# Kernel tuning notes

Hardware: AMD Instinct MI355X
Metric: run time of the kernel (lower is better)

Reference implementation:

```python
import jax, jax.numpy as jnp
import numpy as np

B, N, D = 16, 2048, 1024   # batch, num_windows, input_dim
H, A = 256, 128            # feature head dim, attention hidden dim
EPS = 1e-5                 # torch LayerNorm eps
NEG = -1e9                 # finite mask value (avoids NaN in softmax/grads)
KMAX = max(1, N // 10)     # static upper bound on per-sample top-k


def setup_inputs() -> dict:
    key = jax.random.key(0)
    ks = jax.random.split(key, 6)
    rn = lambda k, shape, sc: jax.random.normal(k, shape, jnp.float32) * sc
    return {
        "x": rn(ks[0], (B, N, D), 1.0),
        "lengths": jax.random.randint(ks[1], (B,), 0, N, dtype=jnp.int64)
                   if jax.config.jax_enable_x64 else
                   jax.random.randint(ks[1], (B,), 0, N, dtype=jnp.int32),
        # feature_head: Linear(D,H) + LayerNorm(H) (+ GELU, dropout=eval no-op)
        "W1": rn(ks[2], (H, D), D ** -0.5), "b1": jnp.zeros((H,), jnp.float32),
        "ln_g": jnp.ones((H,), jnp.float32), "ln_b": jnp.zeros((H,), jnp.float32),
        # attention: Linear(H,A) -> tanh -> Linear(A,1)
        "Wa1": rn(ks[3], (A, H), H ** -0.5), "ba1": jnp.zeros((A,), jnp.float32),
        "Wa2": rn(ks[4], (1, A), A ** -0.5), "ba2": jnp.zeros((1,), jnp.float32),
        # classifier: Linear(H,1)
        "Wc": rn(ks[5], (1, H), H ** -0.5), "bc": jnp.zeros((1,), jnp.float32),
    }


def reference(x, lengths, W1, b1, ln_g, ln_b, Wa1, ba1, Wa2, ba2, Wc, bc):
    # feature head: Linear + LayerNorm + exact GELU (dropout is identity in eval)
    h = jnp.einsum('bnd,hd->bnh', x, W1) + b1
    mu = h.mean(-1, keepdims=True)
    var = h.var(-1, keepdims=True)  # biased, as in torch LayerNorm
    h = (h - mu) * jax.lax.rsqrt(var + EPS) * ln_g + ln_b
    h = jax.nn.gelu(h, approximate=False)

    instance_scores = jnp.einsum('bnh,oh->bno', h, Wc)[..., 0] + bc[0]   # (B, N)
    a_hidden = jnp.tanh(jnp.einsum('bnh,ah->bna', h, Wa1) + ba1)
    attn_logits = jnp.einsum('bna,oa->bno', a_hidden, Wa2)[..., 0] + ba2[0]  # (B, N)

    T = lengths                                    # (B,)
    mask = jnp.arange(N)[None, :] < T[:, None]     # (B, N) valid-window mask

    # masked softmax attention pooling over the first T windows
    w = jax.nn.softmax(jnp.where(mask, attn_logits, NEG), axis=1)
    attn_score = jnp.sum(w * instance_scores * mask, axis=1)

    # dynamic top-k: k = max(1, floor(0.1*T)); take static KMAX then mask ranks
    k_i = jnp.maximum(1, T // 10)                  # (B,)
    vals, _ = jax.lax.top_k(jnp.where(mask, instance_scores, NEG), KMAX)
    rank_mask = jnp.arange(KMAX)[None, :] < k_i[:, None]
    topk_mean = jnp.sum(vals * rank_mask, axis=1) / k_i.astype(vals.dtype)

    video = jnp.where(T > 0, 0.5 * attn_score + 0.5 * topk_mean,
                      jnp.zeros((), vals.dtype))
    return video[:, None], instance_scores
```

## Files before the change

kernel.cpp:

```cpp
#include <hip/hip_runtime.h>
#include <hip/hip_bf16.h>
#include <cmath>

#define Bn 16
#define Nn 2048
#define Dn 1024
#define Hn 256
#define An 128

typedef __bf16 bf16x8 __attribute__((ext_vector_type(8)));
typedef float f32x4 __attribute__((ext_vector_type(4)));
typedef unsigned short ushort8v __attribute__((ext_vector_type(8)));
typedef unsigned int uint4v __attribute__((ext_vector_type(4)));

#define LDS_BARRIER do {                                   \
    asm volatile("s_waitcnt lgkmcnt(0)" ::: "memory");     \
    __builtin_amdgcn_s_barrier();                          \
    __builtin_amdgcn_sched_barrier(0);                     \
  } while (0)

static __device__ __forceinline__ unsigned short f2bf(float f) {
  unsigned u = __float_as_uint(f);
  u += 0x7fffu + ((u >> 16) & 1u);
  return (unsigned short)(u >> 16);
}

static __device__ __forceinline__ bf16x8 cvt8(const float4 a, const float4 b) {
  bf16x8 r;
  r[0] = (__bf16)a.x; r[1] = (__bf16)a.y; r[2] = (__bf16)a.z; r[3] = (__bf16)a.w;
  r[4] = (__bf16)b.x; r[5] = (__bf16)b.y; r[6] = (__bf16)b.z; r[7] = (__bf16)b.w;
  return r;
}

__global__ __launch_bounds__(256) void pack_weights(
    const float* __restrict__ W1, const float* __restrict__ Wa1,
    unsigned short* __restrict__ w1p, unsigned short* __restrict__ wa1p) {
  const int idx = blockIdx.x * 256 + threadIdx.x;
  const float* src;
  unsigned short* dst;
  if (blockIdx.x < 128) {
    const int kc  = idx >> 10;
    const int u   = idx & 1023;
    const int col = u >> 2;
    const int lq  = (u & 3) ^ ((col >> 1) & 3);
    src = W1 + (size_t)col * Dn + (kc << 5) + (lq << 3);
    dst = w1p + (size_t)idx * 8;
  } else {
    const int v   = idx - 32768;
    const int row = v >> 5;
    const int ls  = (v & 31) ^ (row & 7);
    src = Wa1 + (size_t)row * Hn + (ls << 3);
    dst = wa1p + (size_t)v * 8;
  }
  const float4 a = *(const float4*)src;
  const float4 b = *(const float4*)(src + 4);
  ushort8v o;
  o[0] = f2bf(a.x); o[1] = f2bf(a.y); o[2] = f2bf(a.z); o[3] = f2bf(a.w);
  o[4] = f2bf(b.x); o[5] = f2bf(b.y); o[6] = f2bf(b.z); o[7] = f2bf(b.w);
  *(ushort8v*)dst = o;
}

#define K1A(p) ((p) * 4096)
#define K1B(p) (8192 + (p) * 16384)
#define K1H    8192
#define K1RED  40960
__global__ __launch_bounds__(256, 3) void gemm_ln_kernel(
    const float* __restrict__ x,
    const float* __restrict__ b1,
    const float* __restrict__ ln_g,
    const float* __restrict__ ln_b,
    const float* __restrict__ Wc,
    const float* __restrict__ bc,
    const unsigned short* __restrict__ w1p,
    float* __restrict__ scores_out,
    unsigned short* __restrict__ h_out)
{
  __shared__ __align__(16) char lds[43008];

  const int tid  = threadIdx.x;
  const int wv   = tid >> 6;
  const int lane = tid & 63;
  const int l15  = lane & 15;
  const int lhi  = lane >> 4;
  const int rg   = wv >> 1;
  const int cw   = wv & 1;

  const int gr0 = blockIdx.x << 6;
  const int bb  = gr0 >> 11;
  const int n0  = gr0 & (Nn - 1);

  f32x4 acc[2][8];
  #pragma unroll
  for (int rf = 0; rf < 2; ++rf)
    #pragma unroll
    for (int cf = 0; cf < 8; ++cf)
      acc[rf][cf] = (f32x4){0.f, 0.f, 0.f, 0.f};

  const int arow = tid >> 2, aq = tid & 3;
  const int aphys = aq ^ ((arow >> 1) & 3);
  const float* xsrc = x + (size_t)(gr0 + arow) * Dn + (aq << 3);
  const int awoff = arow * 64 + (aphys << 4);

  const unsigned short* bsrc = w1p + (size_t)tid * 8;

  const int bx    = lhi ^ ((l15 >> 1) & 3);
  const int aoff  = ((rg << 5) + l15) * 64 + (bx << 4);
  const int boff  = (((cw << 7) + l15) * 64) + (bx << 4);

  float4 xs0, xs1;
  uint4v Bst[4];

  auto loadStage = [&](int kc) {
    xs0 = *(const float4*)(xsrc + (kc << 5));
    xs1 = *(const float4*)(xsrc + (kc << 5) + 4);
    const unsigned short* bp = bsrc + (size_t)kc * 8192;
    #pragma unroll
    for (int q = 0; q < 4; ++q)
      Bst[q] = *(const uint4v*)(bp + q * 2048);
  };
  auto writeStage = [&](int p) {
    *(bf16x8*)(lds + K1A(p) + awoff) = cvt8(xs0, xs1);
    #pragma unroll
    for (int q = 0; q < 4; ++q)
      *(uint4v*)(lds + K1B(p) + ((q << 8) + tid) * 16) = Bst[q];
  };
  auto computeStep = [&](int p) {
    const char* Ab = lds + K1A(p);
    const char* Bb = lds + K1B(p);
    __builtin_amdgcn_s_setprio(1);
    const bf16x8 aA = *(const bf16x8*)(Ab + aoff);
    const bf16x8 aB = *(const bf16x8*)(Ab + aoff + 1024);
    #pragma unroll
    for (int cf = 0; cf < 8; ++cf) {
      const bf16x8 bfr = *(const bf16x8*)(Bb + boff + cf * 1024);
      acc[0][cf] = __builtin_amdgcn_mfma_f32_16x16x32_bf16(aA, bfr, acc[0][cf], 0, 0, 0);
      acc[1][cf] = __builtin_amdgcn_mfma_f32_16x16x32_bf16(aB, bfr, acc[1][cf], 0, 0, 0);
    }
    __builtin_amdgcn_s_setprio(0);
  };

  loadStage(0);
  writeStage(0);
  LDS_BARRIER;

  #pragma unroll
  for (int kc = 0; kc < 32; ++kc) {
    const int p = kc & 1;
    if (kc < 31) loadStage(kc + 1);
    computeStep(p);
    if (kc < 31) {
      writeStage(p ^ 1);
      LDS_BARRIER;
    }
  }
  __syncthreads();

  float (*red)[8] = (float(*)[8])(lds + K1RED);

  const float bc0 = bc[0];
  float b1v[8];
  #pragma unroll
  for (int cf = 0; cf < 8; ++cf) b1v[cf] = b1[(cw << 7) + (cf << 4) + l15];

  float ps[2][4], ps2[2][4];
  #pragma unroll
  for (int rf = 0; rf < 2; ++rf)
    #pragma unroll
    for (int r = 0; r < 4; ++r) { ps[rf][r] = 0.f; ps2[rf][r] = 0.f; }

  #pragma unroll
  for (int rf = 0; rf < 2; ++rf)
    #pragma unroll
    for (int cf = 0; cf < 8; ++cf)
      #pragma unroll
      for (int r = 0; r < 4; ++r) {
        const float v = acc[rf][cf][r] + b1v[cf];
        acc[rf][cf][r] = v;
        ps[rf][r] += v; ps2[rf][r] += v * v;
      }
  #pragma unroll
  for (int rf = 0; rf < 2; ++rf)
    #pragma unroll
    for (int r = 0; r < 4; ++r)
      #pragma unroll
      for (int s = 1; s < 16; s <<= 1) {
        ps[rf][r]  += __shfl_xor(ps[rf][r],  s, 64);
        ps2[rf][r] += __shfl_xor(ps2[rf][r], s, 64);
      }
  if (l15 == 0) {
    #pragma unroll
    for (int rf = 0; rf < 2; ++rf)
      #pragma unroll
      for (int r = 0; r < 4; ++r) {
        const int rowb = (rg << 5) + (rf << 4) + (lhi << 2) + r;
        red[rowb][cw << 1]       = ps[rf][r];
        red[rowb][(cw << 1) + 1] = ps2[rf][r];
      }
  }
  __syncthreads();

  float mu[2][4], inv[2][4];
  #pragma unroll
  for (int rf = 0; rf < 2; ++rf)
    #pragma unroll
    for (int r = 0; r < 4; ++r) {
      const int rowb = (rg << 5) + (rf << 4) + (lhi << 2) + r;
      const float s = red[rowb][0] + red[rowb][2];
      const float q = red[rowb][1] + red[rowb][3];
      const float m = s * (1.f / 256.f);
      const float var = q * (1.f / 256.f) - m * m;
      mu[rf][r] = m;
      inv[rf][r] = rsqrtf(var + 1e-5f);
    }

  float gv[8], bv[8], wcv[8];
  #pragma unroll
  for (int cf = 0; cf < 8; ++cf) {
    const int col = (cw << 7) + (cf << 4) + l15;
    gv[cf] = ln_g[col]; bv[cf] = ln_b[col]; wcv[cf] = Wc[col];
  }
  float sc[2][4];
  #pragma unroll
  for (int rf = 0; rf < 2; ++rf)
    #pragma unroll
    for (int r = 0; r < 4; ++r) sc[rf][r] = 0.f;

  #pragma unroll
  for (int rf = 0; rf < 2; ++rf)
    #pragma unroll
    for (int cf = 0; cf < 8; ++cf)
      #pragma unroll
      for (int r = 0; r < 4; ++r) {
        float v = (acc[rf][cf][r] - mu[rf][r]) * inv[rf][r] * gv[cf] + bv[cf];
        v = 0.5f * v * (1.f + erff(v * 0.70710678118654752f));
        sc[rf][r] += v * wcv[cf];
        const int rowb = (rg << 5) + (rf << 4) + (lhi << 2) + r;
        const int col  = (cw << 7) + (cf << 4) + l15;
        *(__bf16*)(lds + K1H + rowb * 512 + (((col >> 3) ^ (rowb & 7)) << 4)
                   + ((col & 7) << 1)) = (__bf16)v;
      }
  #pragma unroll
  for (int rf = 0; rf < 2; ++rf)
    #pragma unroll
    for (int r = 0; r < 4; ++r)
      #pragma unroll
      for (int s = 1; s < 16; s <<= 1)
        sc[rf][r] += __shfl_xor(sc[rf][r], s, 64);
  if (l15 == 0) {
    #pragma unroll
    for (int rf = 0; rf < 2; ++rf)
      #pragma unroll
      for (int r = 0; r < 4; ++r) {
        const int rowb = (rg << 5) + (rf << 4) + (lhi << 2) + r;
        red[rowb][4 + cw] = sc[rf][r];
      }
  }
  __syncthreads();
  if (tid < 64)
    scores_out[(size_t)bb * Nn + n0 + tid] = red[tid][4] + red[tid][5] + bc0;

  #pragma unroll
  for (int j = 0; j < 8; ++j) {
    const int g   = (j << 8) + tid;
    const int row = g >> 5;
    const int c   = g & 31;
    const bf16x8 hv = *(const bf16x8*)(lds + K1H + row * 512 +
                                       ((c ^ (row & 7)) << 4));
    *(bf16x8*)(h_out + (size_t)(gr0 + row) * 256 + (c << 3)) = hv;
  }
}

__global__ __launch_bounds__(512) void stage2_kernel(
    const unsigned short* __restrict__ h_in,
    const unsigned short* __restrict__ wa1p,
    const float* __restrict__ ba1,
    const float* __restrict__ Wa2,
    const float* __restrict__ ba2,
    float* __restrict__ logits_out)
{
  __shared__ __align__(16) char lds2[65536];

  const int tid  = threadIdx.x;
  const int wv   = tid >> 6;
  const int lane = tid & 63;
  const int l15  = lane & 15;
  const int lhi  = lane >> 4;

  const int gr0 = blockIdx.x << 7;
  const int bb  = gr0 >> 11;
  const int n0  = gr0 & (Nn - 1);

  {
    uint4v st[8];
    #pragma unroll
    for (int j = 0; j < 8; ++j)
      st[j] = *(const uint4v*)(wa1p + (size_t)((j << 9) + tid) * 8);
    #pragma unroll
    for (int j = 0; j < 8; ++j)
      *(uint4v*)(lds2 + ((j << 9) + tid) * 16) = st[j];
  }
  __syncthreads();

  f32x4 acc2[8];
  #pragma unroll
  for (int cf = 0; cf < 8; ++cf) acc2[cf] = (f32x4){0.f, 0.f, 0.f, 0.f};

  const unsigned short* hrow = h_in + (size_t)(gr0 + (wv << 4) + l15) * 256 + (lhi << 3);
  #pragma unroll
  for (int ks = 0; ks < 8; ++ks) {
    const bf16x8 af = *(const bf16x8*)(hrow + (ks << 5));
    #pragma unroll
    for (int cf = 0; cf < 8; ++cf) {
      const int row2 = (cf << 4) + l15;
      const bf16x8 bfr = *(const bf16x8*)(lds2 + row2 * 512 +
                          ((((ks << 2) + lhi) ^ (row2 & 7)) << 4));
      acc2[cf] = __builtin_amdgcn_mfma_f32_16x16x32_bf16(af, bfr, acc2[cf], 0, 0, 0);
    }
  }
  const float ba20 = ba2[0];
  float lg[4] = {0.f, 0.f, 0.f, 0.f};
  #pragma unroll
  for (int cf = 0; cf < 8; ++cf) {
    const int col = (cf << 4) + l15;
    const float bav = ba1[col], w2v = Wa2[col];
    #pragma unroll
    for (int r = 0; r < 4; ++r) {
      const float t = acc2[cf][r] + bav;
      const float e = __expf(2.f * t);
      const float th = 1.f - 2.f / (e + 1.f);
      lg[r] += th * w2v;
    }
  }
  #pragma unroll
  for (int r = 0; r < 4; ++r)
    #pragma unroll
    for (int s = 1; s < 16; s <<= 1) lg[r] += __shfl_xor(lg[r], s, 64);
  if (l15 == 0) {
    #pragma unroll
    for (int r = 0; r < 4; ++r)
      logits_out[(size_t)bb * Nn + n0 + (wv << 4) + (lhi << 2) + r] = lg[r] + ba20;
  }
}

__global__ __launch_bounds__(256) void finalize_kernel(
    const int* __restrict__ lengths,
    const float* __restrict__ scores,
    const float* __restrict__ logits,
    float* __restrict__ video)
{
  const int b = blockIdx.x;
  const int tid = threadIdx.x;
  __shared__ float sS[Nn];
  __shared__ float sL[Nn];
  __shared__ unsigned skey[Nn];
  __shared__ float sred[8];

  const int T = lengths[b];
  for (int i = tid; i < Nn; i += 256) {
    sS[i] = scores[(size_t)b * Nn + i];
    sL[i] = logits[(size_t)b * Nn + i];
  }
  __syncthreads();
  if (T <= 0) { if (tid == 0) video[b] = 0.f; return; }

  float m = -3.0e38f;
  for (int i = tid; i < T; i += 256) m = fmaxf(m, sL[i]);
  #pragma unroll
  for (int s = 1; s < 64; s <<= 1) m = fmaxf(m, __shfl_xor(m, s, 64));
  if ((tid & 63) == 0) sred[tid >> 6] = m;
  __syncthreads();
  m = fmaxf(fmaxf(sred[0], sred[1]), fmaxf(sred[2], sred[3]));
  __syncthreads();

  float se = 0.f, swe = 0.f;
  for (int i = tid; i < T; i += 256) {
    const float e = expf(sL[i] - m);
    se += e; swe += e * sS[i];
  }
  #pragma unroll
  for (int s = 1; s < 64; s <<= 1) { se += __shfl_xor(se, s, 64); swe += __shfl_xor(swe, s, 64); }
  if ((tid & 63) == 0) { sred[tid >> 6] = se; sred[4 + (tid >> 6)] = swe; }
  __syncthreads();
  se  = sred[0] + sred[1] + sred[2] + sred[3];
  swe = sred[4] + sred[5] + sred[6] + sred[7];
  __syncthreads();
  const float attn = swe / se;

  for (int i = tid; i < T; i += 256) {
    const unsigned u = __float_as_uint(sS[i]);
    skey[i] = (u & 0x80000000u) ? ~u : (u | 0x80000000u);
  }
  __syncthreads();
  const int k = max(1, T / 10);
  unsigned ans = 0u;
  for (int bit = 31; bit >= 0; --bit) {
    const unsigned cand = ans | (1u << bit);
    int c = 0;
    for (int i = tid; i < T; i += 256) c += (skey[i] >= cand) ? 1 : 0;
    #pragma unroll
    for (int s = 1; s < 64; s <<= 1) c += __shfl_xor(c, s, 64);
    if ((tid & 63) == 0) sred[tid >> 6] = (float)c;
    __syncthreads();
    c = (int)(sred[0] + sred[1] + sred[2] + sred[3]);
    __syncthreads();
    if (c >= k) ans = cand;
  }
  int cgt = 0; float sgt = 0.f;
  for (int i = tid; i < T; i += 256) {
    if (skey[i] > ans) { cgt++; sgt += sS[i]; }
  }
  #pragma unroll
  for (int s = 1; s < 64; s <<= 1) { cgt += __shfl_xor(cgt, s, 64); sgt += __shfl_xor(sgt, s, 64); }
  if ((tid & 63) == 0) { sred[tid >> 6] = (float)cgt; sred[4 + (tid >> 6)] = sgt; }
  __syncthreads();
  cgt = (int)(sred[0] + sred[1] + sred[2] + sred[3]);
  sgt = sred[4] + sred[5] + sred[6] + sred[7];

  const unsigned ub = (ans & 0x80000000u) ? (ans ^ 0x80000000u) : ~ans;
  const float kth = __uint_as_float(ub);
  const float topk = (sgt + (float)(k - cgt) * kth) / (float)k;
  if (tid == 0) video[b] = 0.5f * attn + 0.5f * topk;
}

extern "C" void kernel_launch(void* const* d_in, const int* in_sizes, int n_in,
                              void* d_out, int out_size, void* d_ws, size_t ws_size,
                              hipStream_t stream) {
  const float* x    = (const float*)d_in[0];
  const int*   len  = (const int*)  d_in[1];
  const float* W1   = (const float*)d_in[2];
  const float* b1   = (const float*)d_in[3];
  const float* ln_g = (const float*)d_in[4];
  const float* ln_b = (const float*)d_in[5];
  const float* Wa1  = (const float*)d_in[6];
  const float* ba1  = (const float*)d_in[7];
  const float* Wa2  = (const float*)d_in[8];
  const float* ba2  = (const float*)d_in[9];
  const float* Wc   = (const float*)d_in[10];
  const float* bc   = (const float*)d_in[11];

  float* out    = (float*)d_out;
  float* video  = out;
  float* scores = out + Bn;

  char* ws = (char*)d_ws;
  float*          logits = (float*)ws;
  unsigned short* h_g    = (unsigned short*)(ws + 131072);
  unsigned short* w1p    = (unsigned short*)(ws + 131072 + 16777216);
  unsigned short* wa1p   = (unsigned short*)(ws + 131072 + 16777216 + 524288);

  hipLaunchKernelGGL(pack_weights, dim3(144), dim3(256), 0, stream, W1, Wa1, w1p, wa1p);
  hipLaunchKernelGGL(gemm_ln_kernel, dim3(Bn * Nn / 64), dim3(256), 0, stream,
                     x, b1, ln_g, ln_b, Wc, bc, w1p, scores, h_g);
  hipLaunchKernelGGL(stage2_kernel, dim3(Bn * Nn / 128), dim3(512), 0, stream,
                     h_g, wa1p, ba1, Wa2, ba2, logits);
  hipLaunchKernelGGL(finalize_kernel, dim3(Bn), dim3(256), 0, stream, len, scores, logits, video);
}
```

Measured before the change: 87.40 us.

## Split GEMM+LayerNorm tile across 8 waves with one row fragment each

The fused GEMM+LayerNorm kernel goes from 256 to 512 threads per 64-row block. Each wave now owns 16 rows by 128 columns instead of 32 by 128, and staging loads are split across twice as many threads with smaller per-thread loads. The aim is to cut accumulator registers per thread so more waves fit per CU and hide global and LDS latency better. In exchange, each loaded A fragment is reused across half as many MFMAs, so LDS traffic per MFMA rises, and the per-k-step barrier now synchronises more waves.

```diff
diff --git a/kernel.cpp b/kernel.cpp
--- a/kernel.cpp
+++ b/kernel.cpp
@@ -9,6 +9,7 @@
 #define An 128
 
 typedef __bf16 bf16x8 __attribute__((ext_vector_type(8)));
+typedef __bf16 bf16x4 __attribute__((ext_vector_type(4)));
 typedef float f32x4 __attribute__((ext_vector_type(4)));
 typedef unsigned short ushort8v __attribute__((ext_vector_type(8)));
 typedef unsigned int uint4v __attribute__((ext_vector_type(4)));
@@ -23,13 +24,6 @@
   unsigned u = __float_as_uint(f);
   u += 0x7fffu + ((u >> 16) & 1u);
   return (unsigned short)(u >> 16);
-}
-
-static __device__ __forceinline__ bf16x8 cvt8(const float4 a, const float4 b) {
-  bf16x8 r;
-  r[0] = (__bf16)a.x; r[1] = (__bf16)a.y; r[2] = (__bf16)a.z; r[3] = (__bf16)a.w;
-  r[4] = (__bf16)b.x; r[5] = (__bf16)b.y; r[6] = (__bf16)b.z; r[7] = (__bf16)b.w;
-  return r;
 }
 
 __global__ __launch_bounds__(256) void pack_weights(
@@ -64,7 +58,7 @@
 #define K1B(p) (8192 + (p) * 16384)
 #define K1H    8192
 #define K1RED  40960
-__global__ __launch_bounds__(256, 3) void gemm_ln_kernel(
+__global__ __launch_bounds__(512, 4) void gemm_ln_kernel(
     const float* __restrict__ x,
     const float* __restrict__ b1,
     const float* __restrict__ ln_g,
@@ -83,58 +77,53 @@
   const int l15  = lane & 15;
   const int lhi  = lane >> 4;
   const int rg   = wv >> 1;
-  const int cw   = wv & 1;
+  const int ch   = wv & 1;
 
   const int gr0 = blockIdx.x << 6;
   const int bb  = gr0 >> 11;
   const int n0  = gr0 & (Nn - 1);
 
-  f32x4 acc[2][8];
-  #pragma unroll
-  for (int rf = 0; rf < 2; ++rf)
-    #pragma unroll
-    for (int cf = 0; cf < 8; ++cf)
-      acc[rf][cf] = (f32x4){0.f, 0.f, 0.f, 0.f};
-
-  const int arow = tid >> 2, aq = tid & 3;
-  const int aphys = aq ^ ((arow >> 1) & 3);
-  const float* xsrc = x + (size_t)(gr0 + arow) * Dn + (aq << 3);
-  const int awoff = arow * 64 + (aphys << 4);
+  f32x4 acc[8];
+  #pragma unroll
+  for (int cf = 0; cf < 8; ++cf) acc[cf] = (f32x4){0.f, 0.f, 0.f, 0.f};
+
+  const int arow = tid >> 3, aslot = tid & 7;
+  const float* xsrc = x + (size_t)(gr0 + arow) * Dn + (aslot << 2);
+  const int awoff = arow * 64 + ((((aslot >> 1) ^ ((arow >> 1) & 3)) << 4)
+                                 | ((aslot & 1) << 3));
 
   const unsigned short* bsrc = w1p + (size_t)tid * 8;
 
-  const int bx    = lhi ^ ((l15 >> 1) & 3);
-  const int aoff  = ((rg << 5) + l15) * 64 + (bx << 4);
-  const int boff  = (((cw << 7) + l15) * 64) + (bx << 4);
-
-  float4 xs0, xs1;
-  uint4v Bst[4];
+  const int arow_r = (rg << 4) + l15;
+  const int aoff   = arow_r * 64 + ((lhi ^ ((arow_r >> 1) & 3)) << 4);
+  const int boff   = (((ch << 7) + l15) * 64) + ((lhi ^ ((l15 >> 1) & 3)) << 4);
+
+  float4 xs;
+  uint4v Bst[2];
 
   auto loadStage = [&](int kc) {
-    xs0 = *(const float4*)(xsrc + (kc << 5));
-    xs1 = *(const float4*)(xsrc + (kc << 5) + 4);
+    xs = *(const float4*)(xsrc + (kc << 5));
     const unsigned short* bp = bsrc + (size_t)kc * 8192;
-    #pragma unroll
-    for (int q = 0; q < 4; ++q)
-      Bst[q] = *(const uint4v*)(bp + q * 2048);
+    Bst[0] = *(const uint4v*)(bp);
+    Bst[1] = *(const uint4v*)(bp + 4096);
   };
   auto writeStage = [&](int p) {
-    *(bf16x8*)(lds + K1A(p) + awoff) = cvt8(xs0, xs1);
-    #pragma unroll
-    for (int q = 0; q < 4; ++q)
-      *(uint4v*)(lds + K1B(p) + ((q << 8) + tid) * 16) = Bst[q];
+    bf16x4 t;
+    t[0] = (__bf16)xs.x; t[1] = (__bf16)xs.y;
+    t[2] = (__bf16)xs.z; t[3] = (__bf16)xs.w;
+    *(bf16x4*)(lds + K1A(p) + awoff) = t;
+    *(uint4v*)(lds + K1B(p) + tid * 16) = Bst[0];
+    *(uint4v*)(lds + K1B(p) + 8192 + tid * 16) = Bst[1];
   };
   auto computeStep = [&](int p) {
     const char* Ab = lds + K1A(p);
     const char* Bb = lds + K1B(p);
     __builtin_amdgcn_s_setprio(1);
     const bf16x8 aA = *(const bf16x8*)(Ab + aoff);
-    const bf16x8 aB = *(const bf16x8*)(Ab + aoff + 1024);
     #pragma unroll
     for (int cf = 0; cf < 8; ++cf) {
       const bf16x8 bfr = *(const bf16x8*)(Bb + boff + cf * 1024);
-      acc[0][cf] = __builtin_amdgcn_mfma_f32_16x16x32_bf16(aA, bfr, acc[0][cf], 0, 0, 0);
-      acc[1][cf] = __builtin_amdgcn_mfma_f32_16x16x32_bf16(aB, bfr, acc[1][cf], 0, 0, 0);
+      acc[cf] = __builtin_amdgcn_mfma_f32_16x16x32_bf16(aA, bfr, acc[cf], 0, 0, 0);
     }
     __builtin_amdgcn_s_setprio(0);
   };
@@ -160,108 +149,83 @@
   const float bc0 = bc[0];
   float b1v[8];
   #pragma unroll
-  for (int cf = 0; cf < 8; ++cf) b1v[cf] = b1[(cw << 7) + (cf << 4) + l15];
-
-  float ps[2][4], ps2[2][4];
-  #pragma unroll
-  for (int rf = 0; rf < 2; ++rf)
-    #pragma unroll
-    for (int r = 0; r < 4; ++r) { ps[rf][r] = 0.f; ps2[rf][r] = 0.f; }
-
-  #pragma unroll
-  for (int rf = 0; rf < 2; ++rf)
-    #pragma unroll
-    for (int cf = 0; cf < 8; ++cf)
-      #pragma unroll
-      for (int r = 0; r < 4; ++r) {
-        const float v = acc[rf][cf][r] + b1v[cf];
-        acc[rf][cf][r] = v;
-        ps[rf][r] += v; ps2[rf][r] += v * v;
-      }
-  #pragma unroll
-  for (int rf = 0; rf < 2; ++rf)
-    #pragma unroll
-    for (int r = 0; r < 4; ++r)
-      #pragma unroll
-      for (int s = 1; s < 16; s <<= 1) {
-        ps[rf][r]  += __shfl_xor(ps[rf][r],  s, 64);
-        ps2[rf][r] += __shfl_xor(ps2[rf][r], s, 64);
-      }
+  for (int cf = 0; cf < 8; ++cf) b1v[cf] = b1[(ch << 7) + (cf << 4) + l15];
+
+  float ps[4] = {0, 0, 0, 0}, ps2[4] = {0, 0, 0, 0};
+  #pragma unroll
+  for (int cf = 0; cf < 8; ++cf)
+    #pragma unroll
+    for (int r = 0; r < 4; ++r) {
+      const float v = acc[cf][r] + b1v[cf];
+      acc[cf][r] = v;
+      ps[r] += v; ps2[r] += v * v;
+    }
+  #pragma unroll
+  for (int r = 0; r < 4; ++r)
+    #pragma unroll
+    for (int s = 1; s < 16; s <<= 1) {
+      ps[r]  += __shfl_xor(ps[r],  s, 64);
+      ps2[r] += __shfl_xor(ps2[r], s, 64);
+    }
   if (l15 == 0) {
     #pragma unroll
-    for (int rf = 0; rf < 2; ++rf)
-      #pragma unroll
-      for (int r = 0; r < 4; ++r) {
-        const int rowb = (rg << 5) + (rf << 4) + (lhi << 2) + r;
-        red[rowb][cw << 1]       = ps[rf][r];
-        red[rowb][(cw << 1) + 1] = ps2[rf][r];
-      }
-  }
-  __syncthreads();
-
-  float mu[2][4], inv[2][4];
-  #pragma unroll
-  for (int rf = 0; rf < 2; ++rf)
-    #pragma unroll
     for (int r = 0; r < 4; ++r) {
-      const int rowb = (rg << 5) + (rf << 4) + (lhi << 2) + r;
-      const float s = red[rowb][0] + red[rowb][2];
-      const float q = red[rowb][1] + red[rowb][3];
-      const float m = s * (1.f / 256.f);
-      const float var = q * (1.f / 256.f) - m * m;
-      mu[rf][r] = m;
-      inv[rf][r] = rsqrtf(var + 1e-5f);
-    }
+      const int rowb = (rg << 4) + (lhi << 2) + r;
+      red[rowb][ch << 1]       = ps[r];
+      red[rowb][(ch << 1) + 1] = ps2[r];
+    }
+  }
+  __syncthreads();
+
+  float mu[4], inv[4];
+  #pragma unroll
+  for (int r = 0; r < 4; ++r) {
+    const int rowb = (rg << 4) + (lhi << 2) + r;
+    const float s = red[rowb][0] + red[rowb][2];
+    const float q = red[rowb][1] + red[rowb][3];
+    const float m = s * (1.f / 256.f);
+    const float var = q * (1.f / 256.f) - m * m;
+    mu[r] = m;
+    inv[r] = rsqrtf(var + 1e-5f);
+  }
 
   float gv[8], bv[8], wcv[8];
   #pragma unroll
   for (int cf = 0; cf < 8; ++cf) {
-    const int col = (cw << 7) + (cf << 4) + l15;
+    const int col = (ch << 7) + (cf << 4) + l15;
     gv[cf] = ln_g[col]; bv[cf] = ln_b[col]; wcv[cf] = Wc[col];
   }
-  float sc[2][4];
-  #pragma unroll
-  for (int rf = 0; rf < 2; ++rf)
-    #pragma unroll
-    for (int r = 0; r < 4; ++r) sc[rf][r] = 0.f;
-
-  #pragma unroll
-  for (int rf = 0; rf < 2; ++rf)
-    #pragma unroll
-    for (int cf = 0; cf < 8; ++cf)
-      #pragma unroll
-      for (int r = 0; r < 4; ++r) {
-        float v = (acc[rf][cf][r] - mu[rf][r]) * inv[rf][r] * gv[cf] + bv[cf];
-        v = 0.5f * v * (1.f + erff(v * 0.70710678118654752f));
-        sc[rf][r] += v * wcv[cf];
-        const int rowb = (rg << 5) + (rf << 4) + (lhi << 2) + r;
-        const int col  = (cw << 7) + (cf << 4) + l15;
-        *(__bf16*)(lds + K1H + rowb * 512 + (((col >> 3) ^ (rowb & 7)) << 4)
-                   + ((col & 7) << 1)) = (__bf16)v;
-      }
-  #pragma unroll
-  for (int rf = 0; rf < 2; ++rf)
-    #pragma unroll
-    for (int r = 0; r < 4; ++r)
-      #pragma unroll
-      for (int s = 1; s < 16; s <<= 1)
-        sc[rf][r] += __shfl_xor(sc[rf][r], s, 64);
+  float sc[4] = {0, 0, 0, 0};
+  #pragma unroll
+  for (int cf = 0; cf < 8; ++cf)
+    #pragma unroll
+    for (int r = 0; r < 4; ++r) {
+      float v = (acc[cf][r] - mu[r]) * inv[r] * gv[cf] + bv[cf];
+      v = 0.5f * v * (1.f + erff(v * 0.70710678118654752f));
+      sc[r] += v * wcv[cf];
+      const int rowb = (rg << 4) + (lhi << 2) + r;
+      const int col  = (ch << 7) + (cf << 4) + l15;
+      *(__bf16*)(lds + K1H + rowb * 512 + (((col >> 3) ^ (rowb & 7)) << 4)
+                 + ((col & 7) << 1)) = (__bf16)v;
+    }
+  #pragma unroll
+  for (int r = 0; r < 4; ++r)
+    #pragma unroll
+    for (int s = 1; s < 16; s <<= 1) sc[r] += __shfl_xor(sc[r], s, 64);
   if (l15 == 0) {
     #pragma unroll
-    for (int rf = 0; rf < 2; ++rf)
-      #pragma unroll
-      for (int r = 0; r < 4; ++r) {
-        const int rowb = (rg << 5) + (rf << 4) + (lhi << 2) + r;
-        red[rowb][4 + cw] = sc[rf][r];
-      }
+    for (int r = 0; r < 4; ++r) {
+      const int rowb = (rg << 4) + (lhi << 2) + r;
+      red[rowb][4 + ch] = sc[r];
+    }
   }
   __syncthreads();
   if (tid < 64)
     scores_out[(size_t)bb * Nn + n0 + tid] = red[tid][4] + red[tid][5] + bc0;
 
   #pragma unroll
-  for (int j = 0; j < 8; ++j) {
-    const int g   = (j << 8) + tid;
+  for (int j = 0; j < 4; ++j) {
+    const int g   = (j << 9) + tid;
     const int row = g >> 5;
     const int c   = g & 31;
     const bf16x8 hv = *(const bf16x8*)(lds + K1H + row * 512 +
@@ -449,7 +413,7 @@
   unsigned short* wa1p   = (unsigned short*)(ws + 131072 + 16777216 + 524288);
 
   hipLaunchKernelGGL(pack_weights, dim3(144), dim3(256), 0, stream, W1, Wa1, w1p, wa1p);
-  hipLaunchKernelGGL(gemm_ln_kernel, dim3(Bn * Nn / 64), dim3(256), 0, stream,
+  hipLaunchKernelGGL(gemm_ln_kernel, dim3(Bn * Nn / 64), dim3(512), 0, stream,
                      x, b1, ln_g, ln_b, Wc, bc, w1p, scores, h_g);
   hipLaunchKernelGGL(stage2_kernel, dim3(Bn * Nn / 128), dim3(512), 0, stream,
                      h_g, wa1p, ba1, Wa2, ba2, logits);
```

After: 88.16 us. About the same (+0.9%).

## Load W1 fragments directly into registers and stage x in larger LDS chunks

Applied to the files above, without the earlier changes.

The GEMM main loop no longer stages the packed W1 tile through LDS. Each wave now loads its bf16 B fragments straight from global memory into registers, double-buffered two k-steps ahead. The x tile is staged in 128-wide k chunks (four MFMA steps per barrier) with an XOR swizzle, which cuts barriers from 31 to 7 and removes B LDS traffic. In exchange register pressure rises, launch bounds drop from 3 to 2 blocks per CU, and W1 reads are duplicated across waves and blocks through cache.

```diff
diff --git a/kernel.cpp b/kernel.cpp
--- a/kernel.cpp
+++ b/kernel.cpp
@@ -60,11 +60,10 @@
   *(ushort8v*)dst = o;
 }
 
-#define K1A(p) ((p) * 4096)
-#define K1B(p) (8192 + (p) * 16384)
-#define K1H    8192
-#define K1RED  40960
-__global__ __launch_bounds__(256, 3) void gemm_ln_kernel(
+#define K1A(p) ((p) * 16384)
+#define K1H    0
+#define K1RED  32768
+__global__ __launch_bounds__(256, 2) void gemm_ln_kernel(
     const float* __restrict__ x,
     const float* __restrict__ b1,
     const float* __restrict__ ln_g,
@@ -75,7 +74,7 @@
     float* __restrict__ scores_out,
     unsigned short* __restrict__ h_out)
 {
-  __shared__ __align__(16) char lds[43008];
+  __shared__ __align__(16) char lds[34816];
 
   const int tid  = threadIdx.x;
   const int wv   = tid >> 6;
@@ -96,61 +95,66 @@
     for (int cf = 0; cf < 8; ++cf)
       acc[rf][cf] = (f32x4){0.f, 0.f, 0.f, 0.f};
 
-  const int arow = tid >> 2, aq = tid & 3;
-  const int aphys = aq ^ ((arow >> 1) & 3);
-  const float* xsrc = x + (size_t)(gr0 + arow) * Dn + (aq << 3);
-  const int awoff = arow * 64 + (aphys << 4);
-
-  const unsigned short* bsrc = w1p + (size_t)tid * 8;
-
-  const int bx    = lhi ^ ((l15 >> 1) & 3);
-  const int aoff  = ((rg << 5) + l15) * 64 + (bx << 4);
-  const int boff  = (((cw << 7) + l15) * 64) + (bx << 4);
-
-  float4 xs0, xs1;
-  uint4v Bst[4];
-
-  auto loadStage = [&](int kc) {
-    xs0 = *(const float4*)(xsrc + (kc << 5));
-    xs1 = *(const float4*)(xsrc + (kc << 5) + 4);
-    const unsigned short* bp = bsrc + (size_t)kc * 8192;
-    #pragma unroll
-    for (int q = 0; q < 4; ++q)
-      Bst[q] = *(const uint4v*)(bp + q * 2048);
+  const int arow = tid >> 2, akq = tid & 3;
+  const float* xsrc = x + (size_t)(gr0 + arow) * Dn + (akq << 5);
+
+  const int ar0 = (rg << 5) + l15;
+  const int ar1 = ar0 + 16;
+  const int axk = l15 & 7;
+
+  const int pq = lhi ^ ((l15 >> 1) & 3);
+  const unsigned short* bbase = w1p + (size_t)(((cw << 7) + l15) << 5) + (pq << 3);
+
+  float4 ast[8];
+  bf16x8 Bpre[2][8];
+
+  auto loadA = [&](int ch) {
+    #pragma unroll
+    for (int j = 0; j < 8; ++j)
+      ast[j] = *(const float4*)(xsrc + (ch << 7) + (j << 2));
   };
-  auto writeStage = [&](int p) {
-    *(bf16x8*)(lds + K1A(p) + awoff) = cvt8(xs0, xs1);
-    #pragma unroll
-    for (int q = 0; q < 4; ++q)
-      *(uint4v*)(lds + K1B(p) + ((q << 8) + tid) * 16) = Bst[q];
+  auto writeA = [&](int p) {
+    #pragma unroll
+    for (int j = 0; j < 4; ++j)
+      *(bf16x8*)(lds + K1A(p) + arow * 256 +
+                 ((((akq << 2) + j) ^ (arow & 7)) << 4)) = cvt8(ast[2 * j], ast[2 * j + 1]);
   };
-  auto computeStep = [&](int p) {
+  auto loadB = [&](bf16x8* dst, int kc) {
+    #pragma unroll
+    for (int cf = 0; cf < 8; ++cf)
+      dst[cf] = *(const bf16x8*)(bbase + (size_t)kc * 8192 + (cf << 9));
+  };
+  auto computeStep = [&](const bf16x8* Bf, int p, int s) {
     const char* Ab = lds + K1A(p);
-    const char* Bb = lds + K1B(p);
+    const int sx = ((((s << 2) + lhi) ^ axk) << 4);
+    const bf16x8 a0 = *(const bf16x8*)(Ab + ar0 * 256 + sx);
+    const bf16x8 a1 = *(const bf16x8*)(Ab + ar1 * 256 + sx);
     __builtin_amdgcn_s_setprio(1);
-    const bf16x8 aA = *(const bf16x8*)(Ab + aoff);
-    const bf16x8 aB = *(const bf16x8*)(Ab + aoff + 1024);
     #pragma unroll
     for (int cf = 0; cf < 8; ++cf) {
-      const bf16x8 bfr = *(const bf16x8*)(Bb + boff + cf * 1024);
-      acc[0][cf] = __builtin_amdgcn_mfma_f32_16x16x32_bf16(aA, bfr, acc[0][cf], 0, 0, 0);
-      acc[1][cf] = __builtin_amdgcn_mfma_f32_16x16x32_bf16(aB, bfr, acc[1][cf], 0, 0, 0);
+      acc[0][cf] = __builtin_amdgcn_mfma_f32_16x16x32_bf16(a0, Bf[cf], acc[0][cf], 0, 0, 0);
+      acc[1][cf] = __builtin_amdgcn_mfma_f32_16x16x32_bf16(a1, Bf[cf], acc[1][cf], 0, 0, 0);
     }
     __builtin_amdgcn_s_setprio(0);
   };
 
-  loadStage(0);
-  writeStage(0);
+  loadA(0);
+  writeA(0);
+  loadB(Bpre[0], 0);
+  loadB(Bpre[1], 1);
   LDS_BARRIER;
+  loadA(1);
 
   #pragma unroll
   for (int kc = 0; kc < 32; ++kc) {
-    const int p = kc & 1;
-    if (kc < 31) loadStage(kc + 1);
-    computeStep(p);
-    if (kc < 31) {
-      writeStage(p ^ 1);
+    const int s  = kc & 3;
+    const int cb = (kc >> 2) & 1;
+    computeStep(Bpre[kc & 1], cb, s);
+    if (kc < 30) loadB(Bpre[kc & 1], kc + 2);
+    if (s == 3 && kc < 31) {
+      writeA(cb ^ 1);
       LDS_BARRIER;
+      if ((kc >> 2) < 6) loadA((kc >> 2) + 2);
     }
   }
   __syncthreads();
```

After: 97.51 us. 11.6% more time.
